# Performance work log

Measured on AMD Instinct MI355X. Metric: run time of the kernel, lower is better.

The kernel has to match this reference:

```python
import jax, jax.numpy as jnp
import numpy as np

N_NODES = 50000
N_EDGES = 625000
N_GRAPHS = 256
CH = 128
N_LAYERS = 3
N_OUT = 10


def setup_inputs() -> dict:
    key = jax.random.key(0)
    ks = jax.random.split(key, 10)
    x = jax.random.normal(ks[0], (N_NODES, CH), dtype=jnp.float32)
    edge_src = jax.random.randint(ks[1], (N_EDGES,), 0, N_NODES, dtype=jnp.int32)
    edge_dst = jax.random.randint(ks[2], (N_EDGES,), 0, N_NODES, dtype=jnp.int32)
    graph_id = jnp.sort(jax.random.randint(ks[3], (N_NODES,), 0, N_GRAPHS, dtype=jnp.int32))
    scale = 0.05
    conv_W = jax.random.normal(ks[4], (N_LAYERS, 3, CH, CH), dtype=jnp.float32) * scale
    conv_b = jnp.zeros((N_LAYERS, 3, CH), dtype=jnp.float32)
    d1_W = jax.random.normal(ks[5], (CH, CH), dtype=jnp.float32) * scale
    d1_b = jnp.zeros((CH,), dtype=jnp.float32)
    d2_W = jax.random.normal(ks[6], (CH, N_OUT), dtype=jnp.float32) * scale
    d2_b = jnp.zeros((N_OUT,), dtype=jnp.float32)
    return dict(x=x, edge_src=edge_src, edge_dst=edge_dst, graph_id=graph_id,
                conv_W=conv_W, conv_b=conv_b, d1_W=d1_W, d1_b=d1_b,
                d2_W=d2_W, d2_b=d2_b)


def _gin_conv(h, edge_src, edge_dst, W, b):
    # aggregate: A @ h via gather + scatter-add (unit edge weights)
    agg = jax.ops.segment_sum(h[edge_src], edge_dst, num_segments=N_NODES)
    # epsilon = 0 -> (1 + eps) * h + agg = h + agg
    z = h + agg
    # MLP: Dense(relu) -> Dense(relu) -> Dense(linear)
    z = jax.nn.relu(z @ W[0] + b[0])
    z = jax.nn.relu(z @ W[1] + b[1])
    z = z @ W[2] + b[2]
    return z


def reference(x, edge_src, edge_dst, graph_id, conv_W, conv_b, d1_W, d1_b, d2_W, d2_b):
    h = x
    for l in range(N_LAYERS):
        h = _gin_conv(h, edge_src, edge_dst, conv_W[l], conv_b[l])
    # GlobalAvgPool over disjoint graphs: segment mean
    sums = jax.ops.segment_sum(h, graph_id, num_segments=N_GRAPHS)
    counts = jax.ops.segment_sum(jnp.ones((h.shape[0],), h.dtype), graph_id,
                                 num_segments=N_GRAPHS)
    pooled = sums / jnp.maximum(counts, 1.0)[:, None]
    h = jax.nn.relu(pooled @ d1_W + d1_b)
    # dropout is identity at inference
    return jax.nn.softmax(h @ d2_W + d2_b, axis=-1)
```

## Files before the change

kernel.cpp:

```cpp
#include <hip/hip_runtime.h>
#include <hip/hip_bf16.h>
#include <math.h>

#define NN 50000
#define NE 625000
#define NG 256
#define CH 128
#define NPAD 50048

typedef __attribute__((ext_vector_type(8))) short short8;
typedef __attribute__((ext_vector_type(4))) float floatx4;

__device__ __forceinline__ float bf2f_lo(unsigned u) {
    union { unsigned i; float f; } c; c.i = u << 16; return c.f;
}
__device__ __forceinline__ float bf2f_hi(unsigned u) {
    union { unsigned i; float f; } c; c.i = u & 0xffff0000u; return c.f;
}
__device__ __forceinline__ float bfu2f(unsigned short us) {
    union { unsigned i; float f; } c; c.i = ((unsigned)us) << 16; return c.f;
}
__device__ __forceinline__ unsigned short f2bfu(float f) {
    __hip_bfloat16 b = __float2bfloat16(f);
    union { __hip_bfloat16 b; unsigned short u; } c; c.b = b; return c.u;
}


__global__ __launch_bounds__(256) void k_hist(const int* __restrict__ dst, int* __restrict__ counts, int n) {
    int e = blockIdx.x * 256 + threadIdx.x;
    if (e < n) atomicAdd(&counts[dst[e]], 1);
}

__global__ __launch_bounds__(256) void k_scan1(const int* __restrict__ counts, int* __restrict__ partial, int n) {
    __shared__ int s[256];
    int t = threadIdx.x;
    int i = blockIdx.x * 256 + t;
    s[t] = (i < n) ? counts[i] : 0;
    __syncthreads();
    for (int d = 128; d > 0; d >>= 1) {
        if (t < d) s[t] += s[t + d];
        __syncthreads();
    }
    if (t == 0) partial[blockIdx.x] = s[0];
}

__global__ __launch_bounds__(256) void k_scan2(const int* __restrict__ partial, int* __restrict__ blockoff, int nb) {
    __shared__ int s[256];
    int t = threadIdx.x;
    int v = (t < nb) ? partial[t] : 0;
    s[t] = v;
    __syncthreads();
    for (int d = 1; d < 256; d <<= 1) {
        int x = (t >= d) ? s[t - d] : 0;
        __syncthreads();
        s[t] += x;
        __syncthreads();
    }
    if (t < nb) blockoff[t] = s[t] - v;
}

__global__ __launch_bounds__(256) void k_scan3(const int* __restrict__ counts, const int* __restrict__ blockoff,
                                               int* __restrict__ offsets, int n) {
    __shared__ int s[256];
    int t = threadIdx.x;
    int i = blockIdx.x * 256 + t;
    int v = (i < n) ? counts[i] : 0;
    s[t] = v;
    __syncthreads();
    for (int d = 1; d < 256; d <<= 1) {
        int x = (t >= d) ? s[t - d] : 0;
        __syncthreads();
        s[t] += x;
        __syncthreads();
    }
    if (i < n) offsets[i] = s[t] - v + blockoff[blockIdx.x];
}

__global__ __launch_bounds__(256) void k_fill(const int* __restrict__ src, const int* __restrict__ dst,
                                              const int* __restrict__ offsets, int* __restrict__ cursor,
                                              int* __restrict__ srclist, int n) {
    int e = blockIdx.x * 256 + threadIdx.x;
    if (e < n) {
        int d = dst[e];
        int pos = atomicAdd(&cursor[d], 1);
        srclist[offsets[d] + pos] = src[e];
    }
}


__global__ __launch_bounds__(256) void k_prep_x(const float* __restrict__ x, unsigned short* __restrict__ hb, int n4) {
    int i = blockIdx.x * 256 + threadIdx.x;
    if (i < n4) {
        float4 v = *(const float4*)&x[i * 4];
        ushort4 o;
        o.x = f2bfu(v.x); o.y = f2bfu(v.y); o.z = f2bfu(v.z); o.w = f2bfu(v.w);
        *(ushort4*)&hb[i * 4] = o;
    }
}

__global__ __launch_bounds__(256) void k_prep_w(const float* __restrict__ W, unsigned short* __restrict__ Wt, int total) {
    int i = blockIdx.x * 256 + threadIdx.x;
    if (i < total) {
        int mat = i >> 14;
        int rem = i & 16383;
        int k = rem >> 7;
        int n = rem & 127;
        Wt[mat * 16384 + n * 128 + k] = f2bfu(W[i]);
    }
}


__global__ __launch_bounds__(256) void k_gather(const unsigned short* __restrict__ h, const int* __restrict__ srclist,
                                                const int* __restrict__ offsets, const int* __restrict__ counts,
                                                unsigned short* __restrict__ outb) {
    int t = threadIdx.x;
    int node = blockIdx.x * 16 + (t >> 4);
    int sub = t & 15;
    int off = offsets[node];
    int deg = counts[node];

    float acc[8];
    {
        uint4 v = *(const uint4*)&h[(size_t)node * CH + sub * 8];
        acc[0] = bf2f_lo(v.x); acc[1] = bf2f_hi(v.x);
        acc[2] = bf2f_lo(v.y); acc[3] = bf2f_hi(v.y);
        acc[4] = bf2f_lo(v.z); acc[5] = bf2f_hi(v.z);
        acc[6] = bf2f_lo(v.w); acc[7] = bf2f_hi(v.w);
    }
#define ACC8(v) \
    acc[0] += bf2f_lo(v.x); acc[1] += bf2f_hi(v.x); \
    acc[2] += bf2f_lo(v.y); acc[3] += bf2f_hi(v.y); \
    acc[4] += bf2f_lo(v.z); acc[5] += bf2f_hi(v.z); \
    acc[6] += bf2f_lo(v.w); acc[7] += bf2f_hi(v.w);
    int i = 0;
    int i0 = 0, i1 = 0, i2 = 0, i3 = 0;
    if (i + 3 < deg) {
        i0 = srclist[off + 0]; i1 = srclist[off + 1];
        i2 = srclist[off + 2]; i3 = srclist[off + 3];
    }
    for (; i + 7 < deg; i += 4) {
        int j0 = srclist[off + i + 4];
        int j1 = srclist[off + i + 5];
        int j2 = srclist[off + i + 6];
        int j3 = srclist[off + i + 7];
        uint4 v0 = *(const uint4*)&h[(size_t)i0 * CH + sub * 8];
        uint4 v1 = *(const uint4*)&h[(size_t)i1 * CH + sub * 8];
        uint4 v2 = *(const uint4*)&h[(size_t)i2 * CH + sub * 8];
        uint4 v3 = *(const uint4*)&h[(size_t)i3 * CH + sub * 8];
        ACC8(v0) ACC8(v1) ACC8(v2) ACC8(v3)
        i0 = j0; i1 = j1; i2 = j2; i3 = j3;
    }
    if (i + 3 < deg) {
        uint4 v0 = *(const uint4*)&h[(size_t)i0 * CH + sub * 8];
        uint4 v1 = *(const uint4*)&h[(size_t)i1 * CH + sub * 8];
        uint4 v2 = *(const uint4*)&h[(size_t)i2 * CH + sub * 8];
        uint4 v3 = *(const uint4*)&h[(size_t)i3 * CH + sub * 8];
        ACC8(v0) ACC8(v1) ACC8(v2) ACC8(v3)
        i += 4;
    }
    for (; i < deg; i++) {
        uint4 v0 = *(const uint4*)&h[(size_t)srclist[off + i] * CH + sub * 8];
        ACC8(v0)
    }
#undef ACC8
    ushort4 o0, o1;
    o0.x = f2bfu(acc[0]); o0.y = f2bfu(acc[1]); o0.z = f2bfu(acc[2]); o0.w = f2bfu(acc[3]);
    o1.x = f2bfu(acc[4]); o1.y = f2bfu(acc[5]); o1.z = f2bfu(acc[6]); o1.w = f2bfu(acc[7]);
    *(ushort4*)&outb[(size_t)node * CH + sub * 8] = o0;
    *(ushort4*)&outb[(size_t)node * CH + sub * 8 + 4] = o1;
}


__global__ __launch_bounds__(256, 2) void k_layer(const unsigned short* __restrict__ A,
                                                  const unsigned short* __restrict__ Wt3,
                                                  const float* __restrict__ bias3,
                                                  unsigned short* __restrict__ outb,
                                                  float* __restrict__ pooled,
                                                  const int* __restrict__ gid,
                                                  int nrows, int poolMode) {
    __shared__ unsigned short buf[2][128 * 128];

    int t = threadIdx.x;
    int wave = t >> 6;
    int lane = t & 63;
    int q = lane >> 4;
    int ml = lane & 15;
    int waveM = (wave >> 1) * 64;
    int waveN = (wave & 1) * 64;
    int rowBase = blockIdx.x * 128;

#pragma unroll
    for (int iter = 0; iter < 8; iter++) {
        int fid = t + iter * 256;
        int row = fid >> 4;
        int c = fid & 15;
        int r = rowBase + row;
        if (r >= nrows) r = nrows - 1;
        uint4 v = *(const uint4*)&A[(size_t)r * CH + c * 8];
        *(uint4*)&buf[0][row * 128 + ((c ^ (row & 15)) << 3)] = v;
    }
    __syncthreads();

    int rd = 0;
    for (int st = 0; st < 3; st++) {
        const unsigned short* Wm = Wt3 + st * 16384;
        const float* bs = bias3 + st * 128;

        floatx4 acc[4][4];
#pragma unroll
        for (int mt = 0; mt < 4; mt++)
#pragma unroll
            for (int nt = 0; nt < 4; nt++) acc[mt][nt] = (floatx4){0.f, 0.f, 0.f, 0.f};

#pragma unroll
        for (int s = 0; s < 4; s++) {
            short8 a[4], b[4];
#pragma unroll
            for (int mt = 0; mt < 4; mt++) {
                int m = waveM + mt * 16 + ml;
                a[mt] = *(const short8*)&Wm[m * 128 + s * 32 + q * 8];
            }
#pragma unroll
            for (int nt = 0; nt < 4; nt++) {
                int node = waveN + nt * 16 + ml;
                b[nt] = *(const short8*)&buf[rd][node * 128 + (((4 * s + q) ^ ml) << 3)];
            }
#pragma unroll
            for (int mt = 0; mt < 4; mt++)
#pragma unroll
                for (int nt = 0; nt < 4; nt++)
                    acc[mt][nt] = __builtin_amdgcn_mfma_f32_16x16x32_bf16(a[mt], b[nt], acc[mt][nt], 0, 0, 0);
        }

        int wr = rd ^ 1;
        int relu = (st < 2);
        int cw_base = (waveM >> 3);
#pragma unroll
        for (int mt = 0; mt < 4; mt++) {
            float4 bv = *(const float4*)&bs[waveM + mt * 16 + q * 4];
            float bva[4] = {bv.x, bv.y, bv.z, bv.w};
#pragma unroll
            for (int nt = 0; nt < 4; nt++) {
                int node = waveN + nt * 16 + ml;
                ushort4 o;
                float v0 = acc[mt][nt][0] + bva[0];
                float v1 = acc[mt][nt][1] + bva[1];
                float v2 = acc[mt][nt][2] + bva[2];
                float v3 = acc[mt][nt][3] + bva[3];
                if (relu) {
                    v0 = v0 > 0.f ? v0 : 0.f;
                    v1 = v1 > 0.f ? v1 : 0.f;
                    v2 = v2 > 0.f ? v2 : 0.f;
                    v3 = v3 > 0.f ? v3 : 0.f;
                }
                o.x = f2bfu(v0); o.y = f2bfu(v1); o.z = f2bfu(v2); o.w = f2bfu(v3);
                int cw = (cw_base + 2 * mt + (q >> 1)) ^ ml;
                *(ushort4*)&buf[wr][node * 128 + (cw << 3) + (q & 1) * 4] = o;
            }
        }
        __syncthreads();
        rd = wr;
    }

    if (!poolMode) {
#pragma unroll
        for (int iter = 0; iter < 8; iter++) {
            int fid = t + iter * 256;
            int row = fid >> 4;
            int c = fid & 15;
            int r = rowBase + row;
            if (r < nrows) {
                uint4 v = *(const uint4*)&buf[rd][row * 128 + ((c ^ (row & 15)) << 3)];
                *(uint4*)&outb[(size_t)r * CH + c * 8] = v;
            }
        }
    } else {
        int c = t & 127;
        int half = t >> 7;
        int n0 = half * 64;
        float runsum = 0.f;
        int curg = -1;
        for (int n = n0; n < n0 + 64; n++) {
            int r = rowBase + n;
            if (r >= nrows) break;
            int g = gid[r];
            unsigned short u = buf[rd][n * 128 + ((((c >> 3) ^ (n & 15))) << 3) + (c & 7)];
            float v = bfu2f(u);
            if (g != curg) {
                if (curg >= 0) atomicAdd(&pooled[(size_t)curg * CH + c], runsum);
                curg = g;
                runsum = 0.f;
            }
            runsum += v;
        }
        if (curg >= 0) atomicAdd(&pooled[(size_t)curg * CH + c], runsum);
    }
}


__device__ int lowerb(const int* a, int n, int key) {
    int lo = 0, hi = n;
    while (lo < hi) {
        int mid = (lo + hi) >> 1;
        if (a[mid] < key) lo = mid + 1;
        else hi = mid;
    }
    return lo;
}

__global__ __launch_bounds__(128) void k_head(const float* __restrict__ pooled, const int* __restrict__ gid,
                                              const float* __restrict__ W1, const float* __restrict__ b1,
                                              const float* __restrict__ W2, const float* __restrict__ b2,
                                              float* __restrict__ out) {
    __shared__ float p[CH];
    __shared__ float h1[CH];
    __shared__ float lg[10];
    __shared__ int bounds[2];
    int b = blockIdx.x;
    int c = threadIdx.x;
    if (c == 0) bounds[0] = lowerb(gid, NN, b);
    if (c == 1) bounds[1] = lowerb(gid, NN, b + 1);
    __syncthreads();
    float cnt = (float)(bounds[1] - bounds[0]);
    if (cnt < 1.f) cnt = 1.f;
    p[c] = pooled[b * CH + c] / cnt;
    __syncthreads();
    float acc = b1[c];
    for (int k = 0; k < CH; k++) acc += p[k] * W1[k * CH + c];
    h1[c] = acc > 0.f ? acc : 0.f;
    __syncthreads();
    if (c < 10) {
        float a = b2[c];
        for (int k = 0; k < CH; k++) a += h1[k] * W2[k * 10 + c];
        lg[c] = a;
    }
    __syncthreads();
    if (c == 0) {
        float m = lg[0];
        for (int o = 1; o < 10; o++) m = fmaxf(m, lg[o]);
        float e[10];
        float s = 0.f;
        for (int o = 0; o < 10; o++) {
            e[o] = expf(lg[o] - m);
            s += e[o];
        }
        for (int o = 0; o < 10; o++) out[b * 10 + o] = e[o] / s;
    }
}


extern "C" void kernel_launch(void* const* d_in, const int* in_sizes, int n_in,
                              void* d_out, int out_size, void* d_ws, size_t ws_size,
                              hipStream_t stream) {
    const float* x    = (const float*)d_in[0];
    const int* esrc   = (const int*)d_in[1];
    const int* edst   = (const int*)d_in[2];
    const int* gid    = (const int*)d_in[3];
    const float* convW = (const float*)d_in[4];
    const float* convb = (const float*)d_in[5];
    const float* d1W  = (const float*)d_in[6];
    const float* d1b  = (const float*)d_in[7];
    const float* d2W  = (const float*)d_in[8];
    const float* d2b  = (const float*)d_in[9];
    float* out = (float*)d_out;

    char* ws = (char*)d_ws;
    size_t off = 0;
    auto alloc = [&](size_t bytes) -> void* {
        void* p = ws + off;
        off += (bytes + 255) & ~(size_t)255;
        return p;
    };
    unsigned short* hb = (unsigned short*)alloc((size_t)NPAD * CH * 2);
    unsigned short* gb = (unsigned short*)alloc((size_t)NPAD * CH * 2);

    unsigned short* Wt = (unsigned short*)alloc((size_t)9 * 128 * 128 * 2);
    int* counts   = (int*)alloc((size_t)NN * 4);
    int* cursor   = (int*)alloc((size_t)NN * 4);
    int* offs     = (int*)alloc((size_t)NN * 4);
    int* srclist  = (int*)alloc((size_t)NE * 4);
    int* partial  = (int*)alloc(256 * 4);
    int* blockoff = (int*)alloc(256 * 4);
    float* pooled = (float*)alloc((size_t)NG * CH * 4);

    size_t ccBytes = (size_t)((char*)offs - (char*)counts);
    hipMemsetAsync(counts, 0, ccBytes, stream);
    hipMemsetAsync(pooled, 0, (size_t)NG * CH * 4, stream);

    k_hist<<<(NE + 255) / 256, 256, 0, stream>>>(edst, counts, NE);
    int nb = (NN + 255) / 256;
    k_scan1<<<nb, 256, 0, stream>>>(counts, partial, NN);
    k_scan2<<<1, 256, 0, stream>>>(partial, blockoff, nb);
    k_scan3<<<nb, 256, 0, stream>>>(counts, blockoff, offs, NN);
    k_fill<<<(NE + 255) / 256, 256, 0, stream>>>(esrc, edst, offs, cursor, srclist, NE);

    k_prep_x<<<(NN * CH / 4 + 255) / 256, 256, 0, stream>>>(x, hb, NN * CH / 4);
    k_prep_w<<<(9 * 128 * 128 + 255) / 256, 256, 0, stream>>>(convW, Wt, 9 * 128 * 128);

    int nblkL = (NN + 127) / 128;
    for (int l = 0; l < 3; l++) {
        k_gather<<<NN / 16, 256, 0, stream>>>(hb, srclist, offs, counts, gb);
        k_layer<<<nblkL, 256, 0, stream>>>(gb, Wt + (size_t)l * 3 * 16384, convb + l * 3 * CH,
                                           hb, pooled, gid, NN, (l == 2) ? 1 : 0);
    }
    k_head<<<NG, 128, 0, stream>>>(pooled, gid, d1W, d1b, d2W, d2b, out);
}
```

Before: 316.0 us.

## Merge setup kernels into one launch and prefetch next-stage weight fragments

```diff
diff --git a/kernel.cpp b/kernel.cpp
--- a/kernel.cpp
+++ b/kernel.cpp
@@ -8,6 +8,11 @@
 #define CH 128
 #define NPAD 50048
 
+#define NB_HIST 2442
+#define NB_PX   6250
+#define NB_PW   576
+#define NB_PZ   128
+
 typedef __attribute__((ext_vector_type(8))) short short8;
 typedef __attribute__((ext_vector_type(4))) float floatx4;
 
@@ -26,10 +31,34 @@
 }
 
 
-__global__ __launch_bounds__(256) void k_hist(const int* __restrict__ dst, int* __restrict__ counts, int n) {
-    int e = blockIdx.x * 256 + threadIdx.x;
-    if (e < n) atomicAdd(&counts[dst[e]], 1);
-}
+__global__ __launch_bounds__(256) void k_setup(const int* __restrict__ edst, int* __restrict__ counts,
+                                               const float* __restrict__ x, unsigned short* __restrict__ hb,
+                                               const float* __restrict__ convW, unsigned short* __restrict__ Wt,
+                                               float* __restrict__ pooled) {
+    int b = blockIdx.x;
+    int t = threadIdx.x;
+    if (b < NB_HIST) {
+        int e = b * 256 + t;
+        if (e < NE) atomicAdd(&counts[edst[e]], 1);
+    } else if (b < NB_HIST + NB_PX) {
+        int i = (b - NB_HIST) * 256 + t;
+        float4 v = *(const float4*)&x[i * 4];
+        ushort4 o;
+        o.x = f2bfu(v.x); o.y = f2bfu(v.y); o.z = f2bfu(v.z); o.w = f2bfu(v.w);
+        *(ushort4*)&hb[i * 4] = o;
+    } else if (b < NB_HIST + NB_PX + NB_PW) {
+        int i = (b - NB_HIST - NB_PX) * 256 + t;
+        int mat = i >> 14;
+        int rem = i & 16383;
+        int k = rem >> 7;
+        int n = rem & 127;
+        Wt[mat * 16384 + n * 128 + k] = f2bfu(convW[i]);
+    } else {
+        int i = (b - NB_HIST - NB_PX - NB_PW) * 256 + t;
+        pooled[i] = 0.f;
+    }
+}
+
 
 __global__ __launch_bounds__(256) void k_scan1(const int* __restrict__ counts, int* __restrict__ partial, int n) {
     __shared__ int s[256];
@@ -84,28 +113,6 @@
         int d = dst[e];
         int pos = atomicAdd(&cursor[d], 1);
         srclist[offsets[d] + pos] = src[e];
-    }
-}
-
-
-__global__ __launch_bounds__(256) void k_prep_x(const float* __restrict__ x, unsigned short* __restrict__ hb, int n4) {
-    int i = blockIdx.x * 256 + threadIdx.x;
-    if (i < n4) {
-        float4 v = *(const float4*)&x[i * 4];
-        ushort4 o;
-        o.x = f2bfu(v.x); o.y = f2bfu(v.y); o.z = f2bfu(v.z); o.w = f2bfu(v.w);
-        *(ushort4*)&hb[i * 4] = o;
-    }
-}
-
-__global__ __launch_bounds__(256) void k_prep_w(const float* __restrict__ W, unsigned short* __restrict__ Wt, int total) {
-    int i = blockIdx.x * 256 + threadIdx.x;
-    if (i < total) {
-        int mat = i >> 14;
-        int rem = i & 16383;
-        int k = rem >> 7;
-        int n = rem & 127;
-        Wt[mat * 16384 + n * 128 + k] = f2bfu(W[i]);
     }
 }
 
@@ -189,6 +196,13 @@
     int waveN = (wave & 1) * 64;
     int rowBase = blockIdx.x * 128;
 
+    short8 aPre[4];
+#pragma unroll
+    for (int mt = 0; mt < 4; mt++) {
+        int m = waveM + mt * 16 + ml;
+        aPre[mt] = *(const short8*)&Wt3[m * 128 + q * 8];
+    }
+
 #pragma unroll
     for (int iter = 0; iter < 8; iter++) {
         int fid = t + iter * 256;
@@ -217,8 +231,12 @@
             short8 a[4], b[4];
 #pragma unroll
             for (int mt = 0; mt < 4; mt++) {
-                int m = waveM + mt * 16 + ml;
-                a[mt] = *(const short8*)&Wm[m * 128 + s * 32 + q * 8];
+                if (s == 0) {
+                    a[mt] = aPre[mt];
+                } else {
+                    int m = waveM + mt * 16 + ml;
+                    a[mt] = *(const short8*)&Wm[m * 128 + s * 32 + q * 8];
+                }
             }
 #pragma unroll
             for (int nt = 0; nt < 4; nt++) {
@@ -230,6 +248,15 @@
 #pragma unroll
                 for (int nt = 0; nt < 4; nt++)
                     acc[mt][nt] = __builtin_amdgcn_mfma_f32_16x16x32_bf16(a[mt], b[nt], acc[mt][nt], 0, 0, 0);
+        }
+
+        if (st < 2) {
+            const unsigned short* Wn = Wt3 + (st + 1) * 16384;
+#pragma unroll
+            for (int mt = 0; mt < 4; mt++) {
+                int m = waveM + mt * 16 + ml;
+                aPre[mt] = *(const short8*)&Wn[m * 128 + q * 8];
+            }
         }
 
         int wr = rd ^ 1;
@@ -385,18 +412,15 @@
 
     size_t ccBytes = (size_t)((char*)offs - (char*)counts);
     hipMemsetAsync(counts, 0, ccBytes, stream);
-    hipMemsetAsync(pooled, 0, (size_t)NG * CH * 4, stream);
-
-    k_hist<<<(NE + 255) / 256, 256, 0, stream>>>(edst, counts, NE);
+
+    k_setup<<<NB_HIST + NB_PX + NB_PW + NB_PZ, 256, 0, stream>>>(edst, counts, x, hb, convW, Wt, pooled);
+
     int nb = (NN + 255) / 256;
     k_scan1<<<nb, 256, 0, stream>>>(counts, partial, NN);
     k_scan2<<<1, 256, 0, stream>>>(partial, blockoff, nb);
     k_scan3<<<nb, 256, 0, stream>>>(counts, blockoff, offs, NN);
     k_fill<<<(NE + 255) / 256, 256, 0, stream>>>(esrc, edst, offs, cursor, srclist, NE);
 
-    k_prep_x<<<(NN * CH / 4 + 255) / 256, 256, 0, stream>>>(x, hb, NN * CH / 4);
-    k_prep_w<<<(9 * 128 * 128 + 255) / 256, 256, 0, stream>>>(convW, Wt, 9 * 128 * 128);
-
     int nblkL = (NN + 127) / 128;
     for (int l = 0; l < 3; l++) {
         k_gather<<<NN / 16, 256, 0, stream>>>(hb, srclist, offs, counts, gb);
```

Result: faster. 307.0 us (median of 2 runs) (-2.9%).
